# Optimization experiments

Hardware: AMD Instinct MI355X
Metric: run time of the kernel (lower is better)

## Reference

```python
import jax, jax.numpy as jnp
import numpy as np

B, S_DIM, A_DIM = 8192, 39, 4
D_IN = S_DIM + A_DIM  # 43
F = 1024              # n_features width
E = 8                 # n_experts
C = 10                # n_contexts
N_OUT = 1


def setup_inputs() -> dict:
    key = jax.random.key(0)
    ks = jax.random.split(key, 12)
    inp = {
        "state": jax.random.normal(ks[0], (B, S_DIM), jnp.float32),
        "action": jax.random.normal(ks[1], (B, A_DIM), jnp.float32),
        "c": jax.random.randint(ks[2], (B,), 0, C, jnp.int32),
        # per-expert backbone params (InputLayer+ParallelLayer => E independent MLPs)
        "W0": jax.random.normal(ks[3], (E, D_IN, F), jnp.float32) * 0.05,
        "b0": jnp.zeros((E, F), jnp.float32),
        "W1": jax.random.normal(ks[4], (E, F, F), jnp.float32) * 0.03,
        "b1": jnp.zeros((E, F), jnp.float32),
        # task encoder: Linear(n_contexts -> n_experts, bias=False), weight [E, C]
        "Wte": jax.random.normal(ks[5], (E, C), jnp.float32) * 0.3,
        # per-context output heads: Linear(F -> 1)
        "Wh": jax.random.normal(ks[6], (C, F, N_OUT), jnp.float32) * 0.03,
        "bh": jnp.zeros((C, N_OUT), jnp.float32),
    }
    return inp


def reference(state, action, c, W0, b0, W1, b1, Wte, Wh, bh):
    # mixture weights: one_hot(c) @ Wte^T  ==  Wte[:, c]^T  -> [B, E]
    w = Wte.T[c]                                            # [B, E]
    sa = jnp.concatenate([state, action], axis=1)           # [B, D_IN]
    # per-expert backbone MLP (ReLU after each layer, incl. last since activation='ReLU')
    h = jax.nn.relu(jnp.einsum('bi,eio->ebo', sa, W0) + b0[:, None, :])   # [E, B, F]
    h = jax.nn.relu(jnp.einsum('ebi,eio->ebo', h, W1) + b1[:, None, :])   # [E, B, F]
    feats = jnp.transpose(h, (1, 0, 2))                     # [B, E, F]
    feats = jax.nn.relu(feats)                              # agg_activation[0]
    mixed = jnp.einsum('be,bef->bf', w, feats)              # [B, F]
    mixed = jax.nn.relu(mixed)                              # agg_activation[1]
    # context-routed heads: gather each sample's head params (same math as the
    # unique-context scatter loop in the original)
    q = jnp.einsum('bf,bfo->bo', mixed, Wh[c]) + bh[c]      # [B, 1]
    return jnp.squeeze(q, axis=-1)                          # [B]
```

## Files before the change

### kernel.cpp

```cpp
#include <hip/hip_runtime.h>
#include <hip/hip_bf16.h>
#include <stdint.h>

typedef __attribute__((ext_vector_type(8))) __bf16 bf16x8;
typedef __attribute__((ext_vector_type(4))) float f32x4;

__device__ __forceinline__ unsigned short f2b(float f) {
    return __builtin_bit_cast(unsigned short, __float2bfloat16(f));
}

__device__ __forceinline__ void gload_lds16(const void* g, void* l) {
    __builtin_amdgcn_global_load_lds(
        (__attribute__((address_space(1))) void*)(uintptr_t)g,
        (__attribute__((address_space(3))) void*)l,
        16, 0, 0);
}

#define MFMA16(a, b, c) __builtin_amdgcn_mfma_f32_16x16x32_bf16((a), (b), (c), 0, 0, 0)


__global__ void k_prep_sa(const float* __restrict__ state, const float* __restrict__ action,
                          const int* __restrict__ c, const float* __restrict__ Wte,
                          unsigned short* __restrict__ SA, float* __restrict__ wmix, int B) {
    int b = blockIdx.x * 256 + threadIdx.x;
    if (b >= B) return;
    unsigned short* row = SA + (size_t)b * 64;
#pragma unroll
    for (int i = 0; i < 39; ++i) row[i] = f2b(state[(size_t)b * 39 + i]);
#pragma unroll
    for (int i = 0; i < 4; ++i) row[39 + i] = f2b(action[(size_t)b * 4 + i]);
#pragma unroll
    for (int i = 43; i < 64; ++i) row[i] = 0;
    int ctx = c[b];
#pragma unroll
    for (int e = 0; e < 8; ++e) wmix[(size_t)b * 8 + e] = Wte[e * 10 + ctx];
}

__global__ void k_prep_w0t(const float* __restrict__ W0, unsigned short* __restrict__ W0T) {
    int idx = blockIdx.x * 256 + threadIdx.x;
    int e = idx >> 10, f = idx & 1023;
    unsigned short* dst = W0T + (size_t)idx * 64;
#pragma unroll 1
    for (int k = 0; k < 43; ++k) dst[k] = f2b(W0[((size_t)e * 43 + k) * 1024 + f]);
#pragma unroll
    for (int k = 43; k < 64; ++k) dst[k] = 0;
}

__global__ void k_prep_w1t(const float* __restrict__ W1, unsigned short* __restrict__ W1T) {
    __shared__ float t[64][65];
    int k0 = blockIdx.x * 64, n0 = blockIdx.y * 64, e = blockIdx.z;
    int tid = threadIdx.x;
    int cl = tid & 63;
    int rg = tid >> 6;
    const float* src = W1 + ((size_t)e * 1024 + k0) * 1024 + n0;
#pragma unroll
    for (int i = 0; i < 16; ++i) {
        int kr = rg * 16 + i;
        t[kr][cl] = src[(size_t)kr * 1024 + cl];
    }
    __syncthreads();
    int nl = tid >> 2, kg = tid & 3;
    unsigned short* dst = W1T + ((size_t)e * 1024 + n0 + nl) * 1024 + k0 + kg * 16;
#pragma unroll
    for (int j = 0; j < 16; ++j) dst[j] = f2b(t[kg * 16 + j][nl]);
}

__global__ __launch_bounds__(256, 2)
void k_layer0(const unsigned short* __restrict__ SA,
              const unsigned short* __restrict__ W0T,
              const float* __restrict__ b0,
              unsigned short* __restrict__ H0,
              int Bc, int row0) {
    __shared__ unsigned short As[128 * 64];
    __shared__ unsigned short Bs[128 * 64];
    int bm = blockIdx.x, bn = blockIdx.y, e = blockIdx.z;
    int tid = threadIdx.x, lane = tid & 63;
    int wv = tid >> 6, wr = wv >> 1, wc = wv & 1;
    int l15 = lane & 15, kg = lane >> 4;

    const char* Ag = (const char*)(SA + (size_t)(row0 + bm * 128) * 64);
    const char* Bg = (const char*)(W0T + ((size_t)e * 1024 + bn * 128) * 64);
#pragma unroll
    for (int it = 0; it < 4; ++it) {
        int off = tid * 16 + it * 4096;
        gload_lds16(Ag + off, (char*)As + off);
        gload_lds16(Bg + off, (char*)Bs + off);
    }
    __syncthreads();

    f32x4 acc[4][4];
#pragma unroll
    for (int mi = 0; mi < 4; ++mi)
#pragma unroll
        for (int ni = 0; ni < 4; ++ni) acc[mi][ni] = (f32x4)0.0f;

#pragma unroll
    for (int ks = 0; ks < 2; ++ks) {
        bf16x8 af[4], bv[4];
#pragma unroll
        for (int mi = 0; mi < 4; ++mi)
            af[mi] = *(const bf16x8*)&As[(wr * 64 + mi * 16 + l15) * 64 + ks * 32 + kg * 8];
#pragma unroll
        for (int ni = 0; ni < 4; ++ni)
            bv[ni] = *(const bf16x8*)&Bs[(wc * 64 + ni * 16 + l15) * 64 + ks * 32 + kg * 8];
#pragma unroll
        for (int mi = 0; mi < 4; ++mi)
#pragma unroll
            for (int ni = 0; ni < 4; ++ni)
                acc[mi][ni] = MFMA16(af[mi], bv[ni], acc[mi][ni]);
    }

    float b0v[4];
#pragma unroll
    for (int ni = 0; ni < 4; ++ni)
        b0v[ni] = b0[e * 1024 + bn * 128 + wc * 64 + ni * 16 + l15];
#pragma unroll
    for (int mi = 0; mi < 4; ++mi)
#pragma unroll
        for (int ni = 0; ni < 4; ++ni)
#pragma unroll
            for (int j = 0; j < 4; ++j) {
                int rloc = bm * 128 + wr * 64 + mi * 16 + kg * 4 + j;
                int col = bn * 128 + wc * 64 + ni * 16 + l15;
                float h = fmaxf(acc[mi][ni][j] + b0v[ni], 0.0f);
                H0[((size_t)e * Bc + rloc) * 1024 + col] = f2b(h);
            }
}

__global__ __launch_bounds__(256, 2)
void k_layer1_mix(const unsigned short* __restrict__ H0,
                  const unsigned short* __restrict__ W1T,
                  const float* __restrict__ b1,
                  const float* __restrict__ wmix,
                  float* __restrict__ mixed,
                  int Bc, int row0) {
    __shared__ unsigned short As[128 * 32];
    __shared__ unsigned short Bs[128 * 32];

    int nwg = (Bc / 128) * 8;
    int wg = blockIdx.x;
    int cpx = nwg >> 3;
    int swz = (wg & 7) * cpx + (wg >> 3);
    int bm = swz >> 3, bn = swz & 7;

    int tid = threadIdx.x, lane = tid & 63;
    int wv = tid >> 6, wr = wv >> 1, wc = wv & 1;
    int l15 = lane & 15, kg = lane >> 4;

    int flat0 = tid * 16;
    int flat1 = flat0 + 4096;
    int arow0 = flat0 >> 6, akb0 = flat0 & 63;
    int arow1 = flat1 >> 6, akb1 = flat1 & 63;

    f32x4 mix[4][4];
#pragma unroll
    for (int mi = 0; mi < 4; ++mi)
#pragma unroll
        for (int ni = 0; ni < 4; ++ni) mix[mi][ni] = (f32x4)0.0f;

    for (int e = 0; e < 8; ++e) {
        const char* Ae = (const char*)(H0 + ((size_t)e * Bc + bm * 128) * 1024);
        const char* Be = (const char*)(W1T + ((size_t)e * 1024 + bn * 128) * 1024);

        f32x4 acc[4][4];
#pragma unroll
        for (int mi = 0; mi < 4; ++mi)
#pragma unroll
            for (int ni = 0; ni < 4; ++ni) acc[mi][ni] = (f32x4)0.0f;

        for (int k0 = 0; k0 < 1024; k0 += 32) {
            gload_lds16(Ae + (size_t)arow0 * 2048 + k0 * 2 + akb0, (char*)As + flat0);
            gload_lds16(Ae + (size_t)arow1 * 2048 + k0 * 2 + akb1, (char*)As + flat1);
            gload_lds16(Be + (size_t)arow0 * 2048 + k0 * 2 + akb0, (char*)Bs + flat0);
            gload_lds16(Be + (size_t)arow1 * 2048 + k0 * 2 + akb1, (char*)Bs + flat1);
            __syncthreads();

            bf16x8 af[4], bv[4];
#pragma unroll
            for (int mi = 0; mi < 4; ++mi)
                af[mi] = *(const bf16x8*)&As[(wr * 64 + mi * 16 + l15) * 32 + kg * 8];
#pragma unroll
            for (int ni = 0; ni < 4; ++ni)
                bv[ni] = *(const bf16x8*)&Bs[(wc * 64 + ni * 16 + l15) * 32 + kg * 8];
#pragma unroll
            for (int mi = 0; mi < 4; ++mi)
#pragma unroll
                for (int ni = 0; ni < 4; ++ni)
                    acc[mi][ni] = MFMA16(af[mi], bv[ni], acc[mi][ni]);
            __syncthreads();
        }

        float b1v[4];
#pragma unroll
        for (int ni = 0; ni < 4; ++ni)
            b1v[ni] = b1[e * 1024 + bn * 128 + wc * 64 + ni * 16 + l15];
#pragma unroll
        for (int mi = 0; mi < 4; ++mi) {
#pragma unroll
            for (int j = 0; j < 4; ++j) {
                int rloc = bm * 128 + wr * 64 + mi * 16 + kg * 4 + j;
                float w = wmix[(size_t)(row0 + rloc) * 8 + e];
#pragma unroll
                for (int ni = 0; ni < 4; ++ni) {
                    float h = fmaxf(acc[mi][ni][j] + b1v[ni], 0.0f);
                    mix[mi][ni][j] += w * h;
                }
            }
        }
    }

#pragma unroll
    for (int mi = 0; mi < 4; ++mi)
#pragma unroll
        for (int ni = 0; ni < 4; ++ni)
#pragma unroll
            for (int j = 0; j < 4; ++j) {
                int rloc = bm * 128 + wr * 64 + mi * 16 + kg * 4 + j;
                int col = bn * 128 + wc * 64 + ni * 16 + l15;
                mixed[(size_t)rloc * 1024 + col] = fmaxf(mix[mi][ni][j], 0.0f);
            }
}

__global__ void k_head(const float* __restrict__ mixed, const float* __restrict__ Wh,
                       const float* __restrict__ bh, const int* __restrict__ c,
                       float* __restrict__ q, int Bc, int row0) {
    int row = blockIdx.x * 4 + (threadIdx.x >> 6);
    int lane = threadIdx.x & 63;
    if (row >= Bc) return;
    int grow = row0 + row;
    int ctx = c[grow];
    const float4* m4 = (const float4*)(mixed + (size_t)row * 1024);
    const float4* w4 = (const float4*)(Wh + (size_t)ctx * 1024);
    float s = 0.0f;
#pragma unroll
    for (int i = 0; i < 4; ++i) {
        float4 a = m4[lane + i * 64];
        float4 b = w4[lane + i * 64];
        s += a.x * b.x + a.y * b.y + a.z * b.z + a.w * b.w;
    }
#pragma unroll
    for (int off = 32; off > 0; off >>= 1) s += __shfl_down(s, off);
    if (lane == 0) q[grow] = s + bh[ctx];
}

extern "C" void kernel_launch(void* const* d_in, const int* in_sizes, int n_in,
                              void* d_out, int out_size, void* d_ws, size_t ws_size,
                              hipStream_t stream) {
    const float* state  = (const float*)d_in[0];
    const float* action = (const float*)d_in[1];
    const int*   c      = (const int*)d_in[2];
    const float* W0     = (const float*)d_in[3];
    const float* b0     = (const float*)d_in[4];
    const float* W1     = (const float*)d_in[5];
    const float* b1     = (const float*)d_in[6];
    const float* Wte    = (const float*)d_in[7];
    const float* Wh     = (const float*)d_in[8];
    const float* bh     = (const float*)d_in[9];
    float* q = (float*)d_out;
    int B = in_sizes[2];

    char* p = (char*)d_ws;
    unsigned short* W1T = (unsigned short*)p; p += (size_t)8 * 1024 * 1024 * 2;
    unsigned short* W0T = (unsigned short*)p; p += (size_t)8 * 1024 * 64 * 2;
    unsigned short* SA  = (unsigned short*)p; p += (size_t)B * 64 * 2;
    float* wmix         = (float*)p;          p += (size_t)B * 8 * 4;
    size_t fixed = (size_t)(p - (char*)d_ws);

    int Bc = B;
    while (Bc > 128 && fixed + (size_t)Bc * (8 * 1024 * 2 + 1024 * 4) > ws_size) Bc >>= 1;

    unsigned short* H0 = (unsigned short*)p; p += (size_t)8 * Bc * 1024 * 2;
    float* mixed       = (float*)p;

    k_prep_sa<<<(B + 255) / 256, 256, 0, stream>>>(state, action, c, Wte, SA, wmix, B);
    k_prep_w0t<<<(8 * 1024) / 256, 256, 0, stream>>>(W0, W0T);
    k_prep_w1t<<<dim3(16, 16, 8), 256, 0, stream>>>(W1, W1T);

    for (int row0 = 0; row0 < B; row0 += Bc) {
        int nbm = Bc / 128;
        k_layer0<<<dim3(nbm, 8, 8), 256, 0, stream>>>(SA, W0T, b0, H0, Bc, row0);
        k_layer1_mix<<<nbm * 8, 256, 0, stream>>>(H0, W1T, b1, wmix, mixed, Bc, row0);
        k_head<<<(Bc + 3) / 4, 256, 0, stream>>>(mixed, Wh, bh, c, q, Bc, row0);
    }
}
```

Baseline: 229.7 us.

## Enlarge layer1 tile to 256x128 with double-buffered swizzled LDS pipeline

Rewrites the expert-GEMM-plus-mix kernel to use 512-thread blocks computing 256x128 tiles with K=64 stages. The expert and K loops are flattened into one 128-step loop whose LDS buffers are double-buffered: the next stage's global-to-LDS loads are issued before computing on the current one, using explicit vmcnt waits and barriers. An XOR swizzle on the LDS layout reduces bank conflicts, and mixture weights and biases are preloaded into LDS. The aim is to raise reuse per tile and hide memory latency. The cost is about 108KB of LDS per block, which limits occupancy to one block per CU, and half as many blocks in the grid.

```diff
diff --git a/kernel.cpp b/kernel.cpp
--- a/kernel.cpp
+++ b/kernel.cpp
@@ -127,97 +127,152 @@
             }
 }
 
-__global__ __launch_bounds__(256, 2)
+__global__ __launch_bounds__(512, 2)
 void k_layer1_mix(const unsigned short* __restrict__ H0,
                   const unsigned short* __restrict__ W1T,
                   const float* __restrict__ b1,
                   const float* __restrict__ wmix,
                   float* __restrict__ mixed,
                   int Bc, int row0) {
-    __shared__ unsigned short As[128 * 32];
-    __shared__ unsigned short Bs[128 * 32];
-
-    int nwg = (Bc / 128) * 8;
+    __shared__ unsigned short As[2][256 * 64];
+    __shared__ unsigned short Bs[2][128 * 64];
+    __shared__ float wmixLds[256 * 8];
+    __shared__ float b1Lds[8 * 128];
+
+    int nwg = (Bc / 256) * 8;
     int wg = blockIdx.x;
     int cpx = nwg >> 3;
     int swz = (wg & 7) * cpx + (wg >> 3);
     int bm = swz >> 3, bn = swz & 7;
 
     int tid = threadIdx.x, lane = tid & 63;
-    int wv = tid >> 6, wr = wv >> 1, wc = wv & 1;
+    int wv = tid >> 6;
+    int wr = wv >> 1, wc = wv & 1;
     int l15 = lane & 15, kg = lane >> 4;
 
-    int flat0 = tid * 16;
-    int flat1 = flat0 + 4096;
-    int arow0 = flat0 >> 6, akb0 = flat0 & 63;
-    int arow1 = flat1 >> 6, akb1 = flat1 & 63;
-
-    f32x4 mix[4][4];
+    int tid16 = tid * 16;
+    int aSrc[4], aDst[4], bSrc[2], bDst[2];
+#pragma unroll
+    for (int i = 0; i < 4; ++i) {
+        int flat = tid16 + i * 8192;
+        int row = flat >> 7, colb = flat & 127;
+        aDst[i] = flat;
+        aSrc[i] = row * 2048 + (colb ^ ((row & 7) << 4));
+    }
+#pragma unroll
+    for (int i = 0; i < 2; ++i) {
+        int flat = tid16 + i * 8192;
+        int row = flat >> 7, colb = flat & 127;
+        bDst[i] = flat;
+        bSrc[i] = row * 2048 + (colb ^ ((row & 7) << 4));
+    }
+
+    const char* h0base = (const char*)H0 + (size_t)(bm * 256) * 2048;
+    const char* w1base = (const char*)W1T + (size_t)(bn * 128) * 2048;
+    size_t eAstride = (size_t)Bc * 2048;
+
+    int xsw = (l15 & 7) << 4;
+    int aRow[4], bRow[4];
+#pragma unroll
+    for (int mi = 0; mi < 4; ++mi) aRow[mi] = (wr * 64 + mi * 16 + l15) * 128;
+#pragma unroll
+    for (int ni = 0; ni < 4; ++ni) bRow[ni] = (wc * 64 + ni * 16 + l15) * 128;
+    int kg16 = kg * 16;
+
+    for (int idx = tid; idx < 2048; idx += 512) {
+        int r = idx >> 3, e = idx & 7;
+        wmixLds[idx] = wmix[(size_t)(row0 + bm * 256 + r) * 8 + e];
+    }
+#pragma unroll
+    for (int idx = tid; idx < 1024; idx += 512)
+        b1Lds[idx] = b1[(idx >> 7) * 1024 + bn * 128 + (idx & 127)];
+    __syncthreads();
+
+    f32x4 acc[4][4], mix[4][4];
 #pragma unroll
     for (int mi = 0; mi < 4; ++mi)
 #pragma unroll
-        for (int ni = 0; ni < 4; ++ni) mix[mi][ni] = (f32x4)0.0f;
-
-    for (int e = 0; e < 8; ++e) {
-        const char* Ae = (const char*)(H0 + ((size_t)e * Bc + bm * 128) * 1024);
-        const char* Be = (const char*)(W1T + ((size_t)e * 1024 + bn * 128) * 1024);
-
-        f32x4 acc[4][4];
-#pragma unroll
-        for (int mi = 0; mi < 4; ++mi)
-#pragma unroll
-            for (int ni = 0; ni < 4; ++ni) acc[mi][ni] = (f32x4)0.0f;
-
-        for (int k0 = 0; k0 < 1024; k0 += 32) {
-            gload_lds16(Ae + (size_t)arow0 * 2048 + k0 * 2 + akb0, (char*)As + flat0);
-            gload_lds16(Ae + (size_t)arow1 * 2048 + k0 * 2 + akb1, (char*)As + flat1);
-            gload_lds16(Be + (size_t)arow0 * 2048 + k0 * 2 + akb0, (char*)Bs + flat0);
-            gload_lds16(Be + (size_t)arow1 * 2048 + k0 * 2 + akb1, (char*)Bs + flat1);
-            __syncthreads();
-
+        for (int ni = 0; ni < 4; ++ni) { acc[mi][ni] = (f32x4)0.0f; mix[mi][ni] = (f32x4)0.0f; }
+
+    const int NT = 128;
+
+    auto STAGE = [&](int tt) {
+        int e = tt >> 4;
+        int k0b = (tt & 15) << 7;
+        const char* Ab = h0base + (size_t)e * eAstride + k0b;
+        const char* Bb = w1base + (size_t)e * (1024 * 2048) + k0b;
+        char* Ad = (char*)As[tt & 1];
+        char* Bd = (char*)Bs[tt & 1];
+#pragma unroll
+        for (int i = 0; i < 4; ++i) gload_lds16(Ab + aSrc[i], Ad + aDst[i]);
+#pragma unroll
+        for (int i = 0; i < 2; ++i) gload_lds16(Bb + bSrc[i], Bd + bDst[i]);
+    };
+
+    STAGE(0);
+
+    for (int t = 0; t < NT; ++t) {
+        if (t + 1 < NT) {
+            STAGE(t + 1);
+            asm volatile("s_waitcnt vmcnt(6)\n\ts_barrier" ::: "memory");
+        } else {
+            asm volatile("s_waitcnt vmcnt(0)\n\ts_barrier" ::: "memory");
+        }
+        __builtin_amdgcn_sched_barrier(0);
+
+        const char* Ab = (const char*)As[t & 1];
+        const char* Bb = (const char*)Bs[t & 1];
+
+        __builtin_amdgcn_s_setprio(1);
+#pragma unroll
+        for (int ks = 0; ks < 2; ++ks) {
+            int kb = (ks * 64 + kg16) ^ xsw;
             bf16x8 af[4], bv[4];
 #pragma unroll
-            for (int mi = 0; mi < 4; ++mi)
-                af[mi] = *(const bf16x8*)&As[(wr * 64 + mi * 16 + l15) * 32 + kg * 8];
-#pragma unroll
-            for (int ni = 0; ni < 4; ++ni)
-                bv[ni] = *(const bf16x8*)&Bs[(wc * 64 + ni * 16 + l15) * 32 + kg * 8];
+            for (int mi = 0; mi < 4; ++mi) af[mi] = *(const bf16x8*)(Ab + aRow[mi] + kb);
+#pragma unroll
+            for (int ni = 0; ni < 4; ++ni) bv[ni] = *(const bf16x8*)(Bb + bRow[ni] + kb);
 #pragma unroll
             for (int mi = 0; mi < 4; ++mi)
 #pragma unroll
                 for (int ni = 0; ni < 4; ++ni)
                     acc[mi][ni] = MFMA16(af[mi], bv[ni], acc[mi][ni]);
-            __syncthreads();
         }
-
-        float b1v[4];
+        __builtin_amdgcn_s_setprio(0);
+        __builtin_amdgcn_sched_barrier(0);
+        asm volatile("s_waitcnt lgkmcnt(0)\n\ts_barrier" ::: "memory");
+
+        if ((t & 15) == 15) {
+            int e = t >> 4;
+            float b1v[4];
+#pragma unroll
+            for (int ni = 0; ni < 4; ++ni)
+                b1v[ni] = b1Lds[e * 128 + wc * 64 + ni * 16 + l15];
+#pragma unroll
+            for (int mi = 0; mi < 4; ++mi)
+#pragma unroll
+                for (int j = 0; j < 4; ++j) {
+                    int lrow = wr * 64 + mi * 16 + kg * 4 + j;
+                    float w = wmixLds[lrow * 8 + e];
+#pragma unroll
+                    for (int ni = 0; ni < 4; ++ni) {
+                        float h = fmaxf(acc[mi][ni][j] + b1v[ni], 0.0f);
+                        mix[mi][ni][j] += w * h;
+                        acc[mi][ni][j] = 0.0f;
+                    }
+                }
+        }
+    }
+
+#pragma unroll
+    for (int mi = 0; mi < 4; ++mi)
 #pragma unroll
         for (int ni = 0; ni < 4; ++ni)
-            b1v[ni] = b1[e * 1024 + bn * 128 + wc * 64 + ni * 16 + l15];
-#pragma unroll
-        for (int mi = 0; mi < 4; ++mi) {
 #pragma unroll
             for (int j = 0; j < 4; ++j) {
-                int rloc = bm * 128 + wr * 64 + mi * 16 + kg * 4 + j;
-                float w = wmix[(size_t)(row0 + rloc) * 8 + e];
-#pragma unroll
-                for (int ni = 0; ni < 4; ++ni) {
-                    float h = fmaxf(acc[mi][ni][j] + b1v[ni], 0.0f);
-                    mix[mi][ni][j] += w * h;
-                }
-            }
-        }
-    }
-
-#pragma unroll
-    for (int mi = 0; mi < 4; ++mi)
-#pragma unroll
-        for (int ni = 0; ni < 4; ++ni)
-#pragma unroll
-            for (int j = 0; j < 4; ++j) {
-                int rloc = bm * 128 + wr * 64 + mi * 16 + kg * 4 + j;
+                int lrow = wr * 64 + mi * 16 + kg * 4 + j;
                 int col = bn * 128 + wc * 64 + ni * 16 + l15;
-                mixed[(size_t)rloc * 1024 + col] = fmaxf(mix[mi][ni][j], 0.0f);
+                mixed[(size_t)(bm * 256 + lrow) * 1024 + col] = fmaxf(mix[mi][ni][j], 0.0f);
             }
 }
 
@@ -267,7 +322,7 @@
     size_t fixed = (size_t)(p - (char*)d_ws);
 
     int Bc = B;
-    while (Bc > 128 && fixed + (size_t)Bc * (8 * 1024 * 2 + 1024 * 4) > ws_size) Bc >>= 1;
+    while (Bc > 256 && fixed + (size_t)Bc * (8 * 1024 * 2 + 1024 * 4) > ws_size) Bc >>= 1;
 
     unsigned short* H0 = (unsigned short*)p; p += (size_t)8 * Bc * 1024 * 2;
     float* mixed       = (float*)p;
@@ -277,9 +332,8 @@
     k_prep_w1t<<<dim3(16, 16, 8), 256, 0, stream>>>(W1, W1T);
 
     for (int row0 = 0; row0 < B; row0 += Bc) {
-        int nbm = Bc / 128;
-        k_layer0<<<dim3(nbm, 8, 8), 256, 0, stream>>>(SA, W0T, b0, H0, Bc, row0);
-        k_layer1_mix<<<nbm * 8, 256, 0, stream>>>(H0, W1T, b1, wmix, mixed, Bc, row0);
+        k_layer0<<<dim3(Bc / 128, 8, 8), 256, 0, stream>>>(SA, W0T, b0, H0, Bc, row0);
+        k_layer1_mix<<<(Bc / 256) * 8, 512, 0, stream>>>(H0, W1T, b1, wmix, mixed, Bc, row0);
         k_head<<<(Bc + 3) / 4, 256, 0, stream>>>(mixed, Wh, bh, c, q, Bc, row0);
     }
 }
```

Result: no change. 233.6 us (+1.7%).

## Split layer-1 into pipelined 256x256 GEMM and fused mix+head kernel

Applied to the files above, without the earlier changes.

Replaces the fused layer-1+mix kernel with a 512-thread 256x256-tile GEMM. It uses double-buffered, XOR-swizzled LDS staging, interleaves async loads with MFMA phases, and sets wave priority. Per-expert bf16 H1 is written in a fragment-native layout. A new kernel then does the expert mixing, ReLU and context head in one pass, which removes the fp32 mixed buffer and the separate head kernel. In exchange it adds a bf16 round-trip of the 8-expert H1 tensor through memory and rounds H1 to bf16 before mixing.

```diff
diff --git a/kernel.cpp b/kernel.cpp
--- a/kernel.cpp
+++ b/kernel.cpp
@@ -7,6 +7,9 @@
 
 __device__ __forceinline__ unsigned short f2b(float f) {
     return __builtin_bit_cast(unsigned short, __float2bfloat16(f));
+}
+__device__ __forceinline__ float b2f(unsigned int u) {
+    return __builtin_bit_cast(float, u << 16);
 }
 
 __device__ __forceinline__ void gload_lds16(const void* g, void* l) {
@@ -50,8 +53,7 @@
     __shared__ float t[64][65];
     int k0 = blockIdx.x * 64, n0 = blockIdx.y * 64, e = blockIdx.z;
     int tid = threadIdx.x;
-    int cl = tid & 63;
-    int rg = tid >> 6;
+    int cl = tid & 63, rg = tid >> 6;
     const float* src = W1 + ((size_t)e * 1024 + k0) * 1024 + n0;
 #pragma unroll
     for (int i = 0; i < 16; ++i) {
@@ -127,120 +129,256 @@
             }
 }
 
-__global__ __launch_bounds__(256, 2)
-void k_layer1_mix(const unsigned short* __restrict__ H0,
-                  const unsigned short* __restrict__ W1T,
-                  const float* __restrict__ b1,
-                  const float* __restrict__ wmix,
-                  float* __restrict__ mixed,
-                  int Bc, int row0) {
-    __shared__ unsigned short As[128 * 32];
-    __shared__ unsigned short Bs[128 * 32];
-
-    int nwg = (Bc / 128) * 8;
+__global__ __launch_bounds__(512, 2)
+void k_gemm_h1(const unsigned short* __restrict__ H0,
+               const unsigned short* __restrict__ W1T,
+               const float* __restrict__ b1,
+               uint2* __restrict__ H1F,
+               int Bc, int nbm) {
+    __shared__ unsigned short SH[65536];
+
     int wg = blockIdx.x;
-    int cpx = nwg >> 3;
-    int swz = (wg & 7) * cpx + (wg >> 3);
-    int bm = swz >> 3, bn = swz & 7;
+    int c8 = wg & 7, r = wg >> 3;
+    int bn = r & 3, pg = r >> 2;
+    int pair = c8 + 8 * pg;
+    int e = pair / nbm, bm = pair - e * nbm;
 
     int tid = threadIdx.x, lane = tid & 63;
-    int wv = tid >> 6, wr = wv >> 1, wc = wv & 1;
+    int wv = tid >> 6;
+    int wr = wv >> 2, wc = wv & 3;
     int l15 = lane & 15, kg = lane >> 4;
-
-    int flat0 = tid * 16;
-    int flat1 = flat0 + 4096;
-    int arow0 = flat0 >> 6, akb0 = flat0 & 63;
-    int arow1 = flat1 >> 6, akb1 = flat1 & 63;
-
-    f32x4 mix[4][4];
-#pragma unroll
-    for (int mi = 0; mi < 4; ++mi)
-#pragma unroll
-        for (int ni = 0; ni < 4; ++ni) mix[mi][ni] = (f32x4)0.0f;
-
+    int k0s = (kg * 16) ^ ((l15 & 7) << 4);
+    int k1s = (64 + kg * 16) ^ ((l15 & 7) << 4);
+
+    int flat = tid * 16;
+    int srow = flat >> 7;
+    int scol = (flat & 127) ^ ((srow & 7) << 4);
+
+    const char* h0e = (const char*)H0 + ((size_t)e * Bc + (size_t)bm * 256) * 2048;
+    const char* w1e = (const char*)W1T + ((size_t)e * 1024 + (size_t)bn * 256) * 2048;
+    char* Asb = (char*)SH;
+    char* Bsb = (char*)SH + 65536;
+
+    int aRow[8], bRow[4];
+#pragma unroll
+    for (int m = 0; m < 8; ++m) aRow[m] = (((m >> 2) * 64) + (m & 3) * 16 + l15) * 128;
+#pragma unroll
+    for (int n = 0; n < 4; ++n) bRow[n] = ((wc & 1) * 64 + n * 16 + l15) * 128;
+
+    float b1v[4];
+#pragma unroll
+    for (int n = 0; n < 4; ++n)
+        b1v[n] = b1[e * 1024 + bn * 256 + wc * 64 + n * 16 + l15];
+    asm volatile("s_waitcnt vmcnt(0)" ::: "memory");
+
+    auto STAGE_B2 = [&](int tt) {
+        int k0b = tt << 7;
+        char* dstb = Bsb + (tt & 1) * 32768;
+        const char* s0 = w1e + k0b;
+        gload_lds16(s0 + (size_t)srow * 2048 + scol, dstb + flat);
+        gload_lds16(s0 + (size_t)(srow + 64) * 2048 + scol, dstb + flat + 8192);
+        const char* s1 = w1e + (size_t)128 * 2048 + k0b;
+        gload_lds16(s1 + (size_t)srow * 2048 + scol, dstb + 16384 + flat);
+        gload_lds16(s1 + (size_t)(srow + 64) * 2048 + scol, dstb + 16384 + flat + 8192);
+    };
+    auto STAGE_A2 = [&](int tt) {
+        int k0b = tt << 7;
+        char* dsta = Asb + (tt & 1) * 32768;
+        const char* s0 = h0e + k0b;
+        gload_lds16(s0 + (size_t)srow * 2048 + scol, dsta + flat);
+        gload_lds16(s0 + (size_t)(srow + 64) * 2048 + scol, dsta + flat + 8192);
+        const char* s1 = h0e + (size_t)128 * 2048 + k0b;
+        gload_lds16(s1 + (size_t)srow * 2048 + scol, dsta + 16384 + flat);
+        gload_lds16(s1 + (size_t)(srow + 64) * 2048 + scol, dsta + 16384 + flat + 8192);
+    };
+
+    const int NT = 16;
+
+    STAGE_B2(0); STAGE_A2(0);
+    STAGE_B2(1); STAGE_A2(1);
+    asm volatile("s_waitcnt vmcnt(8)" ::: "memory");
+    __builtin_amdgcn_s_barrier();
+
+    f32x4 acc[8][4];
+#pragma unroll
+    for (int m = 0; m < 8; ++m)
+#pragma unroll
+        for (int n = 0; n < 4; ++n) acc[m][n] = (f32x4)0.0f;
+
+#pragma unroll 1
+    for (int t = 0; t < NT; ++t) {
+        int buf = t & 1;
+        const char* Ab = Asb + (buf * 2 + wr) * 16384;
+        const char* Bb = Bsb + (buf * 2 + (wc >> 1)) * 16384;
+
+        bf16x8 af[4][2], bf0[2][2], bf1[2][2];
+
+#pragma unroll
+        for (int mi = 0; mi < 4; ++mi) {
+            af[mi][0] = *(const bf16x8*)(Ab + aRow[mi] + k0s);
+            af[mi][1] = *(const bf16x8*)(Ab + aRow[mi] + k1s);
+        }
+#pragma unroll
+        for (int ni = 0; ni < 2; ++ni) {
+            bf0[ni][0] = *(const bf16x8*)(Bb + bRow[ni] + k0s);
+            bf0[ni][1] = *(const bf16x8*)(Bb + bRow[ni] + k1s);
+        }
+        __builtin_amdgcn_s_barrier();
+        asm volatile("s_waitcnt lgkmcnt(0)" ::: "memory");
+        __builtin_amdgcn_sched_barrier(0);
+        __builtin_amdgcn_s_setprio(1);
+#pragma unroll
+        for (int k = 0; k < 2; ++k)
+#pragma unroll
+            for (int mi = 0; mi < 4; ++mi)
+#pragma unroll
+                for (int ni = 0; ni < 2; ++ni)
+                    acc[mi][ni] = MFMA16(af[mi][k], bf0[ni][k], acc[mi][ni]);
+        __builtin_amdgcn_s_setprio(0);
+        __builtin_amdgcn_sched_barrier(0);
+        __builtin_amdgcn_s_barrier();
+
+#pragma unroll
+        for (int ni = 0; ni < 2; ++ni) {
+            bf1[ni][0] = *(const bf16x8*)(Bb + bRow[2 + ni] + k0s);
+            bf1[ni][1] = *(const bf16x8*)(Bb + bRow[2 + ni] + k1s);
+        }
+        __builtin_amdgcn_s_barrier();
+        asm volatile("s_waitcnt lgkmcnt(0)" ::: "memory");
+        __builtin_amdgcn_sched_barrier(0);
+        __builtin_amdgcn_s_setprio(1);
+#pragma unroll
+        for (int k = 0; k < 2; ++k)
+#pragma unroll
+            for (int mi = 0; mi < 4; ++mi)
+#pragma unroll
+                for (int ni = 0; ni < 2; ++ni)
+                    acc[mi][2 + ni] = MFMA16(af[mi][k], bf1[ni][k], acc[mi][2 + ni]);
+        __builtin_amdgcn_s_setprio(0);
+        __builtin_amdgcn_sched_barrier(0);
+        __builtin_amdgcn_s_barrier();
+
+#pragma unroll
+        for (int mi = 0; mi < 4; ++mi) {
+            af[mi][0] = *(const bf16x8*)(Ab + aRow[4 + mi] + k0s);
+            af[mi][1] = *(const bf16x8*)(Ab + aRow[4 + mi] + k1s);
+        }
+        if (t + 2 < NT) STAGE_B2(t + 2);
+        __builtin_amdgcn_s_barrier();
+        asm volatile("s_waitcnt lgkmcnt(0)" ::: "memory");
+        __builtin_amdgcn_sched_barrier(0);
+        __builtin_amdgcn_s_setprio(1);
+#pragma unroll
+        for (int k = 0; k < 2; ++k)
+#pragma unroll
+            for (int mi = 0; mi < 4; ++mi)
+#pragma unroll
+                for (int ni = 0; ni < 2; ++ni)
+                    acc[4 + mi][2 + ni] = MFMA16(af[mi][k], bf1[ni][k], acc[4 + mi][2 + ni]);
+        __builtin_amdgcn_s_setprio(0);
+        __builtin_amdgcn_sched_barrier(0);
+        __builtin_amdgcn_s_barrier();
+
+        if (t + 2 < NT) STAGE_A2(t + 2);
+        __builtin_amdgcn_s_barrier();
+        __builtin_amdgcn_sched_barrier(0);
+        __builtin_amdgcn_s_setprio(1);
+#pragma unroll
+        for (int k = 0; k < 2; ++k)
+#pragma unroll
+            for (int mi = 0; mi < 4; ++mi)
+#pragma unroll
+                for (int ni = 0; ni < 2; ++ni)
+                    acc[4 + mi][ni] = MFMA16(af[mi][k], bf0[ni][k], acc[4 + mi][ni]);
+        __builtin_amdgcn_s_setprio(0);
+        __builtin_amdgcn_sched_barrier(0);
+        if (t + 2 < NT)
+            asm volatile("s_waitcnt vmcnt(8)" ::: "memory");
+        else
+            asm volatile("s_waitcnt vmcnt(0)" ::: "memory");
+        __builtin_amdgcn_s_barrier();
+    }
+
+    uint2* h1b = H1F + (size_t)((e * nbm + bm) * 4 + bn) * 16384;
+#pragma unroll
+    for (int m = 0; m < 8; ++m)
+#pragma unroll
+        for (int n = 0; n < 4; ++n) {
+            float v0 = fmaxf(acc[m][n][0] + b1v[n], 0.0f);
+            float v1 = fmaxf(acc[m][n][1] + b1v[n], 0.0f);
+            float v2 = fmaxf(acc[m][n][2] + b1v[n], 0.0f);
+            float v3 = fmaxf(acc[m][n][3] + b1v[n], 0.0f);
+            uint2 u;
+            u.x = (unsigned int)f2b(v0) | ((unsigned int)f2b(v1) << 16);
+            u.y = (unsigned int)f2b(v2) | ((unsigned int)f2b(v3) << 16);
+            h1b[((wv * 8 + m) * 4 + n) * 64 + lane] = u;
+        }
+}
+
+__global__ __launch_bounds__(256)
+void k_mixhead(const uint2* __restrict__ H1F, const float* __restrict__ wmix,
+               const float* __restrict__ Wh, const float* __restrict__ bh,
+               const int* __restrict__ c, float* __restrict__ q,
+               int Bc, int row0, int nbm) {
+    int lane = threadIdx.x & 63;
+    int rg = blockIdx.x * 4 + (threadIdx.x >> 6);
+    int rbase = rg * 4;
+    if (rbase >= Bc) return;
+    int bm = rbase >> 8;
+    int lrow = rbase & 255;
+    int wr = lrow >> 7, m = (lrow >> 4) & 7, kg = (lrow >> 2) & 3;
+    int wc = lane >> 4, l15 = lane & 15;
+
+    float w[4][8];
+#pragma unroll
+    for (int j = 0; j < 4; ++j)
+#pragma unroll
+        for (int e = 0; e < 8; ++e)
+            w[j][e] = wmix[(size_t)(row0 + rbase + j) * 8 + e];
+
+    float acc[4][16];
+#pragma unroll
+    for (int j = 0; j < 4; ++j)
+#pragma unroll
+        for (int s = 0; s < 16; ++s) acc[j][s] = 0.0f;
+
+    int ubase = (((wr * 4 + wc) * 8 + m) * 4) * 64 + kg * 16 + l15;
+
+#pragma unroll 1
     for (int e = 0; e < 8; ++e) {
-        const char* Ae = (const char*)(H0 + ((size_t)e * Bc + bm * 128) * 1024);
-        const char* Be = (const char*)(W1T + ((size_t)e * 1024 + bn * 128) * 1024);
-
-        f32x4 acc[4][4];
-#pragma unroll
-        for (int mi = 0; mi < 4; ++mi)
-#pragma unroll
-            for (int ni = 0; ni < 4; ++ni) acc[mi][ni] = (f32x4)0.0f;
-
-        for (int k0 = 0; k0 < 1024; k0 += 32) {
-            gload_lds16(Ae + (size_t)arow0 * 2048 + k0 * 2 + akb0, (char*)As + flat0);
-            gload_lds16(Ae + (size_t)arow1 * 2048 + k0 * 2 + akb1, (char*)As + flat1);
-            gload_lds16(Be + (size_t)arow0 * 2048 + k0 * 2 + akb0, (char*)Bs + flat0);
-            gload_lds16(Be + (size_t)arow1 * 2048 + k0 * 2 + akb1, (char*)Bs + flat1);
-            __syncthreads();
-
-            bf16x8 af[4], bv[4];
-#pragma unroll
-            for (int mi = 0; mi < 4; ++mi)
-                af[mi] = *(const bf16x8*)&As[(wr * 64 + mi * 16 + l15) * 32 + kg * 8];
-#pragma unroll
-            for (int ni = 0; ni < 4; ++ni)
-                bv[ni] = *(const bf16x8*)&Bs[(wc * 64 + ni * 16 + l15) * 32 + kg * 8];
-#pragma unroll
-            for (int mi = 0; mi < 4; ++mi)
-#pragma unroll
-                for (int ni = 0; ni < 4; ++ni)
-                    acc[mi][ni] = MFMA16(af[mi], bv[ni], acc[mi][ni]);
-            __syncthreads();
-        }
-
-        float b1v[4];
-#pragma unroll
-        for (int ni = 0; ni < 4; ++ni)
-            b1v[ni] = b1[e * 1024 + bn * 128 + wc * 64 + ni * 16 + l15];
-#pragma unroll
-        for (int mi = 0; mi < 4; ++mi) {
-#pragma unroll
-            for (int j = 0; j < 4; ++j) {
-                int rloc = bm * 128 + wr * 64 + mi * 16 + kg * 4 + j;
-                float w = wmix[(size_t)(row0 + rloc) * 8 + e];
-#pragma unroll
-                for (int ni = 0; ni < 4; ++ni) {
-                    float h = fmaxf(acc[mi][ni][j] + b1v[ni], 0.0f);
-                    mix[mi][ni][j] += w * h;
-                }
+        size_t eb = (size_t)(e * nbm + bm) * 4;
+#pragma unroll
+        for (int bn = 0; bn < 4; ++bn) {
+            const uint2* blk = H1F + (eb + bn) * 16384;
+#pragma unroll
+            for (int n = 0; n < 4; ++n) {
+                uint2 u = blk[ubase + n * 64];
+                float v0 = b2f(u.x & 0xffffu), v1 = b2f(u.x >> 16);
+                float v2 = b2f(u.y & 0xffffu), v3 = b2f(u.y >> 16);
+                int s = bn * 4 + n;
+                acc[0][s] += w[0][e] * v0;
+                acc[1][s] += w[1][e] * v1;
+                acc[2][s] += w[2][e] * v2;
+                acc[3][s] += w[3][e] * v3;
             }
         }
     }
 
 #pragma unroll
-    for (int mi = 0; mi < 4; ++mi)
-#pragma unroll
-        for (int ni = 0; ni < 4; ++ni)
-#pragma unroll
-            for (int j = 0; j < 4; ++j) {
-                int rloc = bm * 128 + wr * 64 + mi * 16 + kg * 4 + j;
-                int col = bn * 128 + wc * 64 + ni * 16 + l15;
-                mixed[(size_t)rloc * 1024 + col] = fmaxf(mix[mi][ni][j], 0.0f);
-            }
-}
-
-__global__ void k_head(const float* __restrict__ mixed, const float* __restrict__ Wh,
-                       const float* __restrict__ bh, const int* __restrict__ c,
-                       float* __restrict__ q, int Bc, int row0) {
-    int row = blockIdx.x * 4 + (threadIdx.x >> 6);
-    int lane = threadIdx.x & 63;
-    if (row >= Bc) return;
-    int grow = row0 + row;
-    int ctx = c[grow];
-    const float4* m4 = (const float4*)(mixed + (size_t)row * 1024);
-    const float4* w4 = (const float4*)(Wh + (size_t)ctx * 1024);
-    float s = 0.0f;
-#pragma unroll
-    for (int i = 0; i < 4; ++i) {
-        float4 a = m4[lane + i * 64];
-        float4 b = w4[lane + i * 64];
-        s += a.x * b.x + a.y * b.y + a.z * b.z + a.w * b.w;
-    }
-#pragma unroll
-    for (int off = 32; off > 0; off >>= 1) s += __shfl_down(s, off);
-    if (lane == 0) q[grow] = s + bh[ctx];
+    for (int j = 0; j < 4; ++j) {
+        int grow = row0 + rbase + j;
+        int ctx = c[grow];
+        const float* whp = Wh + (size_t)ctx * 1024;
+        float s = 0.0f;
+#pragma unroll
+        for (int slot = 0; slot < 16; ++slot) {
+            int f = (slot >> 2) * 256 + wc * 64 + (slot & 3) * 16 + l15;
+            s += fmaxf(acc[j][slot], 0.0f) * whp[f];
+        }
+#pragma unroll
+        for (int off = 32; off > 0; off >>= 1) s += __shfl_down(s, off);
+        if (lane == 0) q[grow] = s + bh[ctx];
+    }
 }
 
 extern "C" void kernel_launch(void* const* d_in, const int* in_sizes, int n_in,
@@ -267,19 +405,19 @@
     size_t fixed = (size_t)(p - (char*)d_ws);
 
     int Bc = B;
-    while (Bc > 128 && fixed + (size_t)Bc * (8 * 1024 * 2 + 1024 * 4) > ws_size) Bc >>= 1;
+    while (Bc > 256 && fixed + (size_t)Bc * 32768 > ws_size) Bc >>= 1;
 
     unsigned short* H0 = (unsigned short*)p; p += (size_t)8 * Bc * 1024 * 2;
-    float* mixed       = (float*)p;
+    uint2* H1F         = (uint2*)p;
 
     k_prep_sa<<<(B + 255) / 256, 256, 0, stream>>>(state, action, c, Wte, SA, wmix, B);
     k_prep_w0t<<<(8 * 1024) / 256, 256, 0, stream>>>(W0, W0T);
     k_prep_w1t<<<dim3(16, 16, 8), 256, 0, stream>>>(W1, W1T);
 
     for (int row0 = 0; row0 < B; row0 += Bc) {
-        int nbm = Bc / 128;
-        k_layer0<<<dim3(nbm, 8, 8), 256, 0, stream>>>(SA, W0T, b0, H0, Bc, row0);
-        k_layer1_mix<<<nbm * 8, 256, 0, stream>>>(H0, W1T, b1, wmix, mixed, Bc, row0);
-        k_head<<<(Bc + 3) / 4, 256, 0, stream>>>(mixed, Wh, bh, c, q, Bc, row0);
-    }
-}
+        int nbm = Bc / 256;
+        k_layer0<<<dim3(Bc / 128, 8, 8), 256, 0, stream>>>(SA, W0T, b0, H0, Bc, row0);
+        k_gemm_h1<<<nbm * 32, 512, 0, stream>>>(H0, W1T, b1, H1F, Bc, nbm);
+        k_mixhead<<<Bc / 16, 256, 0, stream>>>(H1F, wmix, Wh, bh, c, q, Bc, row0, nbm);
+    }
+}
```

Measured after the change: 251.6 us. +9.6%, slower.
